# Kernel optimization log

Measured on AMD Instinct MI355X. Metric: run time of the kernel, lower is better.

## Reference

```python
import jax, jax.numpy as jnp
import numpy as np

EMBED_DIM = 1024
NUM_HEADS = 16
HEAD_DIM = EMBED_DIM // NUM_HEADS
SCALING = HEAD_DIM ** -0.5


def setup_inputs() -> dict:
    key = jax.random.key(0)
    ks = jax.random.split(key, 10)
    B, S, D = 2, 2048, EMBED_DIM
    lim = 1.0 / np.sqrt(D)  # torch Linear default init scale
    def lin(k):
        kw, kb = jax.random.split(k)
        W = jax.random.uniform(kw, (D, D), jnp.float32, -lim, lim)
        b = jax.random.uniform(kb, (D,), jnp.float32, -lim, lim)
        return W, b
    Wq, bq = lin(ks[0])
    Wk, bk = lin(ks[1])
    Wv, bv = lin(ks[2])
    Wo, bo = lin(ks[3])
    hidden_states = jax.random.normal(ks[4], (B, S, D), jnp.float32)
    attention_mask = jnp.ones((B, S), jnp.int32)  # unused by the module's forward
    return {"hidden_states": hidden_states, "attention_mask": attention_mask,
            "Wq": Wq, "bq": bq, "Wk": Wk, "bk": bk, "Wv": Wv, "bv": bv,
            "Wo": Wo, "bo": bo}


def reference(hidden_states, attention_mask, Wq, bq, Wk, bk, Wv, bv, Wo, bo):
    B, S, D = hidden_states.shape
    H, hd = NUM_HEADS, HEAD_DIM

    def split_heads(x):  # [B,S,D] -> [B,H,S,hd]
        return x.reshape(B, S, H, hd).transpose(0, 2, 1, 3)

    q = split_heads(hidden_states @ Wq.T + bq) * SCALING
    k = split_heads(hidden_states @ Wk.T + bk)
    v = split_heads(hidden_states @ Wv.T + bv)

    scores = jnp.einsum("bhqd,bhkd->bhqk", q, k)  # [B,H,S,S]
    mask_value = jnp.finfo(scores.dtype).min
    causal = jnp.triu(jnp.ones((S, S), bool), k=1)  # True above diagonal
    scores = jnp.where(causal, mask_value, scores)
    probs = jax.nn.softmax(scores, axis=-1)

    out = jnp.einsum("bhqk,bhkd->bhqd", probs, v)  # [B,H,S,hd]
    out = out.transpose(0, 2, 1, 3).reshape(B, S, D)
    return out @ Wo.T + bo
```

## Files before the change

### kernel.cpp

```cpp
#include <hip/hip_runtime.h>


typedef __bf16 bf16;
typedef __attribute__((ext_vector_type(8))) __bf16 bf16x8;
typedef __attribute__((ext_vector_type(4))) __bf16 bf16x4;
typedef __attribute__((ext_vector_type(4))) float f32x4;

#define MFMA16(a, b, c) __builtin_amdgcn_mfma_f32_16x16x32_bf16((a), (b), (c), 0, 0, 0)

__device__ __forceinline__ void gl_lds16(const bf16* g, bf16* l) {
  __builtin_amdgcn_global_load_lds(
      (__attribute__((address_space(1))) void*)g,
      (__attribute__((address_space(3))) void*)l, 16, 0, 0);
}

__global__ __launch_bounds__(256) void cvt5(
    const float* __restrict__ x, const float* __restrict__ wq,
    const float* __restrict__ wk, const float* __restrict__ wv,
    const float* __restrict__ wo,
    bf16* __restrict__ xb, bf16* __restrict__ wqb, bf16* __restrict__ wkb,
    bf16* __restrict__ wvb, bf16* __restrict__ wob) {
  const int bx = blockIdx.x;
  const float* s;
  bf16* d;
  int base;
  if (bx < 4096)      { s = x;  d = xb;  base = bx; }
  else if (bx < 5120) { s = wq; d = wqb; base = bx - 4096; }
  else if (bx < 6144) { s = wk; d = wkb; base = bx - 5120; }
  else if (bx < 7168) { s = wv; d = wvb; base = bx - 6144; }
  else                { s = wo; d = wob; base = bx - 7168; }
  const int i = base * 1024 + threadIdx.x * 4;
  const float4 v = *(const float4*)(s + i);
  bf16x4 o;
  o[0] = (bf16)v.x; o[1] = (bf16)v.y; o[2] = (bf16)v.z; o[3] = (bf16)v.w;
  *(bf16x4*)(d + i) = o;
}

__global__ __launch_bounds__(256) void vtrans(const bf16* __restrict__ v,
                                              bf16* __restrict__ vt) {
  __shared__ bf16 Ts[64 * 80];
  const int t = threadIdx.x;
  const int st = blockIdx.x;
  const int bh = blockIdx.y;
  const int bb = bh >> 4, h = bh & 15;
  const bf16* src = v + ((size_t)bb * 2048 + st * 64) * 1024 + h * 64;
#pragma unroll
  for (int i = 0; i < 2; ++i) {
    const int idx = i * 256 + t;
    const int sl = idx >> 3, c = idx & 7;
    *(bf16x8*)&Ts[sl * 80 + c * 8] = *(const bf16x8*)(src + (size_t)sl * 1024 + c * 8);
  }
  __syncthreads();
  bf16* dst = vt + (size_t)bh * 64 * 2048 + st * 64;
#pragma unroll
  for (int i = 0; i < 2; ++i) {
    const int idx = i * 256 + t;
    const int d = idx >> 3, c2 = idx & 7;
    bf16x8 tmp;
#pragma unroll
    for (int e = 0; e < 8; ++e) tmp[e] = Ts[(c2 * 8 + e) * 80 + d];
    *(bf16x8*)(dst + (size_t)d * 2048 + c2 * 8) = tmp;
  }
}

template <int BM, typename OutT>
__global__ __launch_bounds__(256, 2) void gemm_bt3(
    const bf16* __restrict__ A,
    const bf16* __restrict__ W0, const bf16* __restrict__ W1, const bf16* __restrict__ W2,
    const float* __restrict__ B0, const float* __restrict__ B1, const float* __restrict__ B2,
    OutT* __restrict__ O0, OutT* __restrict__ O1, OutT* __restrict__ O2,
    float s0, float s1, float s2, int K) {
  constexpr int WM = BM / 32;
  __shared__ bf16 As[BM * 32];
  __shared__ bf16 Bs[128 * 32];

  const int t = threadIdx.x;
  const int lane = t & 63;
  const int wv = t >> 6;
  const int wm = wv & 1, wn = wv >> 1;
  const int qd = lane >> 4, ln = lane & 15;

  const int which = blockIdx.x >> 3;
  const bf16* W = (which == 0) ? W0 : (which == 1) ? W1 : W2;
  const float* Bi = (which == 0) ? B0 : (which == 1) ? B1 : B2;
  OutT* O = (which == 0) ? O0 : (which == 1) ? O1 : O2;
  const float scale = (which == 0) ? s0 : (which == 1) ? s1 : s2;

  const int n0 = (blockIdx.x & 7) * 128;
  const int m0 = blockIdx.y * BM;

  f32x4 acc[WM][4] = {};

  const bf16* ga = A + (size_t)(m0 + (t >> 2)) * K + (t & 3) * 8;
  const bf16* gb = W + (size_t)(n0 + (t >> 2)) * K + (t & 3) * 8;
  bf16* lA = &As[t * 8];
  bf16* lB = &Bs[t * 8];

  for (int k0 = 0; k0 < K; k0 += 32) {
#pragma unroll
    for (int i = 0; i < BM / 64; ++i)
      gl_lds16(ga + (size_t)i * 64 * K + k0, lA + i * 2048);
#pragma unroll
    for (int i = 0; i < 2; ++i)
      gl_lds16(gb + (size_t)i * 64 * K + k0, lB + i * 2048);
    __syncthreads();

    bf16x8 af[WM], bw[4];
#pragma unroll
    for (int i = 0; i < WM; ++i)
      af[i] = *(const bf16x8*)&As[(wm * (BM / 2) + i * 16 + ln) * 32 + qd * 8];
#pragma unroll
    for (int j = 0; j < 4; ++j)
      bw[j] = *(const bf16x8*)&Bs[(wn * 64 + j * 16 + ln) * 32 + qd * 8];
#pragma unroll
    for (int i = 0; i < WM; ++i)
#pragma unroll
      for (int j = 0; j < 4; ++j)
        acc[i][j] = MFMA16(af[i], bw[j], acc[i][j]);
    __syncthreads();
  }

#pragma unroll
  for (int i = 0; i < WM; ++i) {
    const int row = m0 + wm * (BM / 2) + i * 16 + qd * 4;
#pragma unroll
    for (int j = 0; j < 4; ++j) {
      const int col = n0 + wn * 64 + j * 16 + ln;
      const float bias = Bi[col];
#pragma unroll
      for (int r = 0; r < 4; ++r) {
        const float v = (acc[i][j][r] + bias) * scale;
        O[(size_t)(row + r) * 1024 + col] = (OutT)v;
      }
    }
  }
}

__global__ __launch_bounds__(256, 2) void attn_causal(
    const bf16* __restrict__ Q, const bf16* __restrict__ Kg,
    const bf16* __restrict__ VT, bf16* __restrict__ Ob) {
  __shared__ bf16 Ks[2][128 * 64];
  __shared__ bf16 Vts[2][64 * 128];
  __shared__ bf16 Ps[4][16 * 128];

  const int t = threadIdx.x;
  const int lane = t & 63;
  const int w = t >> 6;
  const int qd = lane >> 4, ln = lane & 15;

  const int blk = blockIdx.x;
  const int bh = blk & 31;
  const int pr = blk >> 5;
  const int bb = bh >> 4, h = bh & 15;
  const size_t rowbase = (size_t)bb * 2048;
  const bf16* vtb = VT + (size_t)bh * 64 * 2048;

  auto stage = [&](int buf, int j) {
    const bf16* kp = Kg + (rowbase + j * 128) * 1024 + h * 64;
#pragma unroll
    for (int i = 0; i < 4; ++i) {
      const int s = i * 256 + t;
      const int kv = s >> 3, cp = s & 7;
      const int c = cp ^ (kv & 7);
      gl_lds16(kp + (size_t)kv * 1024 + c * 8, &Ks[buf][s * 8]);
    }
#pragma unroll
    for (int i = 0; i < 4; ++i) {
      const int s = i * 256 + t;
      const int d = s >> 4, cp = s & 15;
      const int c = cp ^ (d & 15);
      gl_lds16(vtb + (size_t)d * 2048 + j * 128 + c * 8, &Vts[buf][s * 8]);
    }
  };

#pragma unroll 1
  for (int pass = 0; pass < 2; ++pass) {
    const int tq = (pass == 0) ? pr : (31 - pr);
    const int q0 = tq * 64;
    const int nj = (tq >> 1) + 1;

    const bf16* qp = Q + (rowbase + q0 + w * 16) * 1024 + h * 64;
    bf16x8 qf[2];
#pragma unroll
    for (int ks = 0; ks < 2; ++ks)
      qf[ks] = *(const bf16x8*)(qp + (size_t)ln * 1024 + ks * 32 + qd * 8);

    float l_run[4] = {0.f, 0.f, 0.f, 0.f};
    f32x4 accO[4] = {};

    __syncthreads();
    stage(0, 0);

#pragma unroll 1
    for (int j = 0; j < nj; ++j) {
      const int buf = j & 1;
      __syncthreads();
      if (j + 1 < nj) stage(buf ^ 1, j + 1);

      f32x4 accS[8] = {};
#pragma unroll
      for (int ks = 0; ks < 2; ++ks) {
#pragma unroll
        for (int nt = 0; nt < 8; ++nt) {
          const bf16x8 bk = *(const bf16x8*)
              &Ks[buf][(nt * 16 + ln) * 64 + (((ks * 4 + qd) ^ (ln & 7)) << 3)];
          accS[nt] = MFMA16(qf[ks], bk, accS[nt]);
        }
      }

      const bool dom = (j == nj - 1);
#pragma unroll
      for (int r = 0; r < 4; ++r) {
        const int row = qd * 4 + r;
        const int qg = q0 + w * 16 + row;
        float sum = 0.f;
#pragma unroll
        for (int nt = 0; nt < 8; ++nt) {
          float p = __expf(accS[nt][r]);
          const int col = nt * 16 + ln;
          if (dom && (j * 128 + col) > qg) p = 0.f;
          sum += p;
          Ps[w][row * 128 + ((((col >> 3) ^ row)) << 3) + (col & 7)] = (bf16)p;
        }
        l_run[r] += sum;
      }

#pragma unroll
      for (int kt = 0; kt < 4; ++kt) {
        const bf16x8 ap = *(const bf16x8*)
            &Ps[w][ln * 128 + (((kt * 4 + qd) ^ ln) << 3)];
#pragma unroll
        for (int nt = 0; nt < 4; ++nt) {
          const bf16x8 bv = *(const bf16x8*)
              &Vts[buf][(nt * 16 + ln) * 128 + (((kt * 4 + qd) ^ ln) << 3)];
          accO[nt] = MFMA16(ap, bv, accO[nt]);
        }
      }
    }

    bf16* op = Ob + (rowbase + q0 + w * 16) * 1024 + h * 64;
#pragma unroll
    for (int r = 0; r < 4; ++r) {
      float l = l_run[r];
#pragma unroll
      for (int off = 1; off < 16; off <<= 1) l += __shfl_xor(l, off, 64);
      const float inv_l = 1.0f / l;
#pragma unroll
      for (int nt = 0; nt < 4; ++nt)
        op[(size_t)(qd * 4 + r) * 1024 + nt * 16 + ln] = (bf16)(accO[nt][r] * inv_l);
    }
  }
}

extern "C" void kernel_launch(void* const* d_in, const int* in_sizes, int n_in,
                              void* d_out, int out_size, void* d_ws, size_t ws_size,
                              hipStream_t stream) {
  const float* X  = (const float*)d_in[0];
  const float* Wq = (const float*)d_in[2];
  const float* bq = (const float*)d_in[3];
  const float* Wk = (const float*)d_in[4];
  const float* bk = (const float*)d_in[5];
  const float* Wv = (const float*)d_in[6];
  const float* bv = (const float*)d_in[7];
  const float* Wo = (const float*)d_in[8];
  const float* bo = (const float*)d_in[9];
  float* out = (float*)d_out;

  bf16* xb  = (bf16*)d_ws;
  bf16* wqb = xb  + (size_t)4096 * 1024;
  bf16* wkb = wqb + (size_t)1024 * 1024;
  bf16* wvb = wkb + (size_t)1024 * 1024;
  bf16* wob = wvb + (size_t)1024 * 1024;
  bf16* q   = wob + (size_t)1024 * 1024;
  bf16* k   = q   + (size_t)4096 * 1024;
  bf16* v   = k   + (size_t)4096 * 1024;
  bf16* vt  = v   + (size_t)4096 * 1024;
  bf16* ao  = xb;

  const float scaling = 0.125f;

  dim3 blk(256);
  cvt5<<<dim3(8192), blk, 0, stream>>>(X, Wq, Wk, Wv, Wo, xb, wqb, wkb, wvb, wob);
  gemm_bt3<128, bf16><<<dim3(24, 32), blk, 0, stream>>>(
      xb, wqb, wkb, wvb, bq, bk, bv, q, k, v, scaling, 1.f, 1.f, 1024);
  vtrans<<<dim3(32, 32), blk, 0, stream>>>(v, vt);
  attn_causal<<<dim3(512), blk, 0, stream>>>(q, k, vt, ao);
  gemm_bt3<64, float><<<dim3(8, 64), blk, 0, stream>>>(
      ao, wob, wob, wob, bo, bo, bo, out, out, out, 1.f, 1.f, 1.f, 1024);
}
```

Measured before the change: 190.5 us.

## Double-buffer GEMM LDS tiles with BK=64 and XOR swizzle

Restructures the projection GEMM main loop to double-buffer LDS tiles, prefetching the next K-slab via global_load_lds while computing the current one. K-step grows from 32 to 64, halving the number of barriers per tile, and an XOR swizzle on the column chunk is meant to cut LDS bank conflicts. Occupancy hint rises to 3 for smaller BM. The cost is more LDS per block, which may limit occupancy.

```diff
diff --git a/kernel.cpp b/kernel.cpp
--- a/kernel.cpp
+++ b/kernel.cpp
@@ -64,15 +64,15 @@
 }
 
 template <int BM, typename OutT>
-__global__ __launch_bounds__(256, 2) void gemm_bt3(
+__global__ __launch_bounds__(256, BM == 128 ? 2 : 3) void gemm_bt3(
     const bf16* __restrict__ A,
     const bf16* __restrict__ W0, const bf16* __restrict__ W1, const bf16* __restrict__ W2,
     const float* __restrict__ B0, const float* __restrict__ B1, const float* __restrict__ B2,
     OutT* __restrict__ O0, OutT* __restrict__ O1, OutT* __restrict__ O2,
     float s0, float s1, float s2, int K) {
   constexpr int WM = BM / 32;
-  __shared__ bf16 As[BM * 32];
-  __shared__ bf16 Bs[128 * 32];
+  __shared__ bf16 As[2][BM * 64];
+  __shared__ bf16 Bs[2][128 * 64];
 
   const int t = threadIdx.x;
   const int lane = t & 63;
@@ -91,33 +91,50 @@
 
   f32x4 acc[WM][4] = {};
 
-  const bf16* ga = A + (size_t)(m0 + (t >> 2)) * K + (t & 3) * 8;
-  const bf16* gb = W + (size_t)(n0 + (t >> 2)) * K + (t & 3) * 8;
-  bf16* lA = &As[t * 8];
-  bf16* lB = &Bs[t * 8];
-
-  for (int k0 = 0; k0 < K; k0 += 32) {
-#pragma unroll
-    for (int i = 0; i < BM / 64; ++i)
-      gl_lds16(ga + (size_t)i * 64 * K + k0, lA + i * 2048);
-#pragma unroll
-    for (int i = 0; i < 2; ++i)
-      gl_lds16(gb + (size_t)i * 64 * K + k0, lB + i * 2048);
+  auto stage = [&](int buf, int k0) {
+#pragma unroll
+    for (int i = 0; i < BM / 32; ++i) {
+      const int s = i * 256 + t;
+      const int row = s >> 3;
+      const int c = (s & 7) ^ (row & 7);
+      gl_lds16(A + (size_t)(m0 + row) * K + k0 + c * 8, &As[buf][s * 8]);
+    }
+#pragma unroll
+    for (int i = 0; i < 4; ++i) {
+      const int s = i * 256 + t;
+      const int row = s >> 3;
+      const int c = (s & 7) ^ (row & 7);
+      gl_lds16(W + (size_t)(n0 + row) * K + k0 + c * 8, &Bs[buf][s * 8]);
+    }
+  };
+
+  const int nit = K >> 6;
+  stage(0, 0);
+#pragma unroll 1
+  for (int it = 0; it < nit; ++it) {
+    const int buf = it & 1;
     __syncthreads();
-
-    bf16x8 af[WM], bw[4];
-#pragma unroll
-    for (int i = 0; i < WM; ++i)
-      af[i] = *(const bf16x8*)&As[(wm * (BM / 2) + i * 16 + ln) * 32 + qd * 8];
-#pragma unroll
-    for (int j = 0; j < 4; ++j)
-      bw[j] = *(const bf16x8*)&Bs[(wn * 64 + j * 16 + ln) * 32 + qd * 8];
-#pragma unroll
-    for (int i = 0; i < WM; ++i)
-#pragma unroll
-      for (int j = 0; j < 4; ++j)
-        acc[i][j] = MFMA16(af[i], bw[j], acc[i][j]);
-    __syncthreads();
+    if (it + 1 < nit) stage(buf ^ 1, (it + 1) * 64);
+
+#pragma unroll
+    for (int ks = 0; ks < 2; ++ks) {
+      bf16x8 af[WM], bw[4];
+#pragma unroll
+      for (int i = 0; i < WM; ++i) {
+        const int r = wm * (BM / 2) + i * 16 + ln;
+        af[i] = *(const bf16x8*)&As[buf][r * 64 + (((ks * 4 + qd) ^ (ln & 7)) << 3)];
+      }
+#pragma unroll
+      for (int j = 0; j < 4; ++j) {
+        const int r = wn * 64 + j * 16 + ln;
+        bw[j] = *(const bf16x8*)&Bs[buf][r * 64 + (((ks * 4 + qd) ^ (ln & 7)) << 3)];
+      }
+#pragma unroll
+      for (int i = 0; i < WM; ++i)
+#pragma unroll
+        for (int j = 0; j < 4; ++j)
+          acc[i][j] = MFMA16(af[i], bw[j], acc[i][j]);
+    }
   }
 
 #pragma unroll
```

Result: no change. 192.6 us (+1.1%).
